# Kernel tuning notes

Hardware: AMD Instinct MI355X
Metric: run time of the kernel (lower is better)

The kernel has to match this reference:

```python
import jax, jax.numpy as jnp
import numpy as np

N_NODES = 40000
N_EDGES = 640000
IN_CH = 64
HID = 128
N_LAYERS = 3


def _linear_params(key, shape_in, shape_out):
    kw, kb = jax.random.split(key)
    lim = 1.0 / np.sqrt(shape_in)
    W = jax.random.uniform(kw, (shape_in, shape_out), jnp.float32, -lim, lim)
    b = jax.random.uniform(kb, (shape_out,), jnp.float32, -lim, lim)
    return W, b


def setup_inputs() -> dict:
    key = jax.random.key(0)
    ks = jax.random.split(key, 32)
    edge_index = jax.random.randint(ks[0], (2, N_EDGES), 0, N_NODES, dtype=jnp.int64 if jax.config.jax_enable_x64 else jnp.int32)
    x = jax.random.normal(ks[1], (N_NODES, IN_CH), jnp.float32)
    pos = jax.random.normal(ks[2], (N_NODES, 3), jnp.float32)
    emb_W, emb_b = _linear_params(ks[3], IN_CH, HID)

    def stack(fn):
        outs = [fn(l) for l in range(N_LAYERS)]
        Ws = jnp.stack([o[0] for o in outs])
        bs = jnp.stack([o[1] for o in outs])
        return Ws, bs

    # edge MLP: Linear(2H+1, H), SiLU, Linear(H, H), SiLU
    edge_W1, edge_b1 = stack(lambda l: _linear_params(ks[4 + l], 2 * HID + 1, HID))
    edge_W2, edge_b2 = stack(lambda l: _linear_params(ks[8 + l], HID, HID))
    # node MLP: Linear(2H, H), SiLU, Linear(H, H)
    node_W1, node_b1 = stack(lambda l: _linear_params(ks[12 + l], 2 * HID, HID))
    node_W2, node_b2 = stack(lambda l: _linear_params(ks[16 + l], HID, HID))
    # pos MLP: Linear(H, H), SiLU, Linear(H, 1)
    pos_W1, pos_b1 = stack(lambda l: _linear_params(ks[20 + l], HID, HID))
    pos_W2, pos_b2 = stack(lambda l: _linear_params(ks[24 + l], HID, 1))
    return {
        "edge_index": edge_index, "x": x, "pos": pos,
        "emb_W": emb_W, "emb_b": emb_b,
        "edge_W1": edge_W1, "edge_b1": edge_b1, "edge_W2": edge_W2, "edge_b2": edge_b2,
        "node_W1": node_W1, "node_b1": node_b1, "node_W2": node_W2, "node_b2": node_b2,
        "pos_W1": pos_W1, "pos_b1": pos_b1, "pos_W2": pos_W2, "pos_b2": pos_b2,
    }


def reference(edge_index, x, pos, emb_W, emb_b,
              edge_W1, edge_b1, edge_W2, edge_b2,
              node_W1, node_b1, node_W2, node_b2,
              pos_W1, pos_b1, pos_W2, pos_b2):
    silu = jax.nn.silu
    N = x.shape[0]
    src, dst = edge_index[0], edge_index[1]  # messages flow src -> dst
    # node embedding
    h = x @ emb_W + emb_b  # [N, H]
    # in-degree for mean aggregation of position updates
    deg = jnp.clip(jax.ops.segment_sum(jnp.ones(src.shape[0], pos.dtype), dst, num_segments=N), 1.0)
    L = edge_W1.shape[0]
    for l in range(L):
        h_i = h[dst]            # [E, H] target features
        h_j = h[src]            # [E, H] source features
        rel = pos[dst] - pos[src]  # [E, 3]
        d2 = jnp.sum(rel * rel, axis=-1, keepdims=True)  # [E, 1] squared distance
        e_in = jnp.concatenate([h_i, h_j, d2], axis=-1)  # [E, 2H+1]
        m = silu(silu(e_in @ edge_W1[l] + edge_b1[l]) @ edge_W2[l] + edge_b2[l])  # [E, H]
        agg = jax.ops.segment_sum(m, dst, num_segments=N)  # [N, H]
        n_in = jnp.concatenate([h, agg], axis=-1)  # [N, 2H]
        h = silu(n_in @ node_W1[l] + node_b1[l]) @ node_W2[l] + node_b2[l]
        # equivariant position update: pos_i += mean_j (pos_i - pos_j) * phi_x(m_ij)
        w = silu(m @ pos_W1[l] + pos_b1[l]) @ pos_W2[l] + pos_b2[l]  # [E, 1]
        pos = pos + jax.ops.segment_sum(rel * w, dst, num_segments=N) / deg[:, None]
    return h, pos
```

## Files before the change

### kernel.cpp

```cpp
#include <hip/hip_runtime.h>
#include <hip/hip_bf16.h>

#define N_NODES 40000
#define N_EDGES 640000
#define IN_CH 64
#define HID 128
#define N_LAYERS 3

typedef unsigned short u16;
typedef unsigned int u32;

typedef __attribute__((ext_vector_type(8))) __bf16 bf16x8;
typedef __attribute__((ext_vector_type(4))) float float4v;

__device__ __forceinline__ float bf2f(u16 u) {
    union { u32 i; float f; } v; v.i = ((u32)u) << 16; return v.f;
}
__device__ __forceinline__ float bflo(u32 p) {
    union { u32 i; float f; } v; v.i = p << 16; return v.f;
}
__device__ __forceinline__ float bfhi(u32 p) {
    union { u32 i; float f; } v; v.i = p & 0xffff0000u; return v.f;
}
__device__ __forceinline__ u16 f2bf(float f) {
    union { float f; u32 i; } v; v.f = f;
    u32 i = v.i;
    u32 r = (i + 0x7fffu + ((i >> 16) & 1u)) >> 16;
    return (u16)r;
}
#if __has_builtin(__builtin_amdgcn_cvt_pk_bf16_f32)
typedef __attribute__((ext_vector_type(2))) __bf16 bf16x2_t;
__device__ __forceinline__ u32 pk2bf(float a, float b) {
    bf16x2_t p = __builtin_amdgcn_cvt_pk_bf16_f32(a, b);
    union { bf16x2_t v; u32 u; } c; c.v = p; return c.u;
}
#else
__device__ __forceinline__ u32 pk2bf(float a, float b) {
    return (u32)f2bf(a) | ((u32)f2bf(b) << 16);
}
#endif
__device__ __forceinline__ float silu_f(float x) {
    float d = 1.0f + __expf(-x);
#if __has_builtin(__builtin_amdgcn_rcpf)
    return x * __builtin_amdgcn_rcpf(d);
#else
    return __fdividef(x, d);
#endif
}

#define W_STRIDE 72
__device__ __forceinline__ void stage_w64(const u16* __restrict__ g, u16* s, int t,
                                          int chunk, int rowstride_u32) {
    const u32* gp = (const u32*)g;
    u32* sp = (u32*)s;
#pragma unroll
    for (int it = 0; it < 4; ++it) {
        int i4 = t + it * 256;
        int n = i4 >> 3, j = i4 & 7;
        *(uint4*)(sp + n * 36 + j * 4) = *(const uint4*)(gp + n * rowstride_u32 + chunk * 32 + j * 4);
    }
}

__global__ void detect_kernel(const void* __restrict__ w_raw,
                              const void* __restrict__ eidx_raw,
                              int* __restrict__ flags) {
    __shared__ int s_big, s_hi;
    if (threadIdx.x == 0) { s_big = 0; s_hi = 0; }
    __syncthreads();
    const u16* w16 = (const u16*)w_raw;
    for (int i = threadIdx.x; i < 8192; i += blockDim.x) {
        float v = bf2f(w16[i]);
        if (!(fabsf(v) <= 1.0f)) s_big = 1;
    }
    const u32* e32 = (const u32*)eidx_raw;
    for (int i = threadIdx.x; i < 256; i += blockDim.x) {
        if (e32[2 * i + 1] != 0u) s_hi = 1;
    }
    __syncthreads();
    if (threadIdx.x == 0) {
        flags[0] = s_big ? 0 : 1;
        flags[1] = s_hi ? 0 : 1;
    }
}

__global__ void small_cvt_kernel(
    const void* __restrict__ embB_raw, const void* __restrict__ eB1_raw,
    const void* __restrict__ eB2_raw, const void* __restrict__ pB1_raw,
    const void* __restrict__ pB2_raw, const void* __restrict__ pW2_raw,
    const void* __restrict__ eW1_raw, const void* __restrict__ nB1_raw,
    const void* __restrict__ nB2_raw,
    float* __restrict__ dstf, const int* __restrict__ flags)
{
    int i = blockIdx.x * blockDim.x + threadIdx.x;
    if (i >= 2820) return;
    const void* src; int si;
    if (i < 128)       { src = embB_raw; si = i; }
    else if (i < 512)  { src = eB1_raw;  si = i - 128; }
    else if (i < 896)  { src = eB2_raw;  si = i - 512; }
    else if (i < 1280) { src = pB1_raw;  si = i - 896; }
    else if (i < 1284) { src = pB2_raw;  si = i - 1280; if (si >= 3) { dstf[i] = 0.f; return; } }
    else if (i < 1668) { src = pW2_raw;  si = i - 1284; }
    else if (i < 2052) { int j = i - 1668; src = eW1_raw; si = (j >> 7) * 32896 + 32768 + (j & 127); }
    else if (i < 2436) { src = nB1_raw;  si = i - 2052; }
    else               { src = nB2_raw;  si = i - 2436; }
    dstf[i] = flags[0] ? bf2f(((const u16*)src)[si]) : ((const float*)src)[si];
}

__global__ void wcvt_kernel(
    const void* __restrict__ eW1_raw, const void* __restrict__ eW2_raw,
    const void* __restrict__ pW1_raw, const void* __restrict__ nW1_raw,
    const void* __restrict__ nW2_raw, const void* __restrict__ embW_raw,
    u16* __restrict__ W1abt, u16* __restrict__ W2t, u16* __restrict__ pW1t,
    u16* __restrict__ nW1t, u16* __restrict__ nW2t, u16* __restrict__ embWt,
    const int* __restrict__ flags)
{
    int z = blockIdx.z, l = blockIdx.y;
    int i = blockIdx.x * blockDim.x + threadIdx.x;
    const void* src; u16* dst; int si, di;
    if (z == 0) {
        if (i >= 32768) return;
        int o = i >> 7, k = i & 127;
        si = l * 32896 + ((o < 128) ? (k * 128 + o) : ((128 + k) * 128 + (o - 128)));
        src = eW1_raw; dst = W1abt; di = l * 32768 + i;
    } else if (z == 1) {
        if (i >= 16384) return;
        int n = i >> 7, k = i & 127;
        si = l * 16384 + k * 128 + n; src = eW2_raw; dst = W2t; di = l * 16384 + i;
    } else if (z == 2) {
        if (i >= 16384) return;
        int n = i >> 7, k = i & 127;
        si = l * 16384 + k * 128 + n; src = pW1_raw; dst = pW1t; di = l * 16384 + i;
    } else if (z == 3) {
        if (i >= 32768) return;
        int n = i >> 8, k = i & 255;
        si = l * 32768 + k * 128 + n; src = nW1_raw; dst = nW1t; di = l * 32768 + i;
    } else if (z == 4) {
        if (i >= 16384) return;
        int n = i >> 7, k = i & 127;
        si = l * 16384 + k * 128 + n; src = nW2_raw; dst = nW2t; di = l * 16384 + i;
    } else {
        if (l != 0 || i >= 8192) return;
        int n = i >> 6, k = i & 63;
        si = k * 128 + n; src = embW_raw; dst = embWt; di = i;
    }
    float v = flags[0] ? bf2f(((const u16*)src)[si]) : ((const float*)src)[si];
    dst[di] = f2bf(v);
}

__global__ void cnt_kernel(const void* __restrict__ eidx, int* __restrict__ cnt,
                           const int* __restrict__ flags) {
    int e = blockIdx.x * blockDim.x + threadIdx.x;
    if (e >= N_EDGES) return;
    int dn = flags[1] ? (int)((const long long*)eidx)[N_EDGES + e]
                      : ((const int*)eidx)[N_EDGES + e];
    atomicAdd(&cnt[dn], 1);
}

__global__ __launch_bounds__(1024) void scan_kernel(const int* __restrict__ cnt,
                                                    int* __restrict__ offs) {
    __shared__ int s_part[1024];
    const int t = threadIdx.x;
    const int base = t * 40;
    int sum = 0;
    for (int j = 0; j < 40; ++j) {
        int idx = base + j;
        sum += (idx < N_NODES) ? cnt[idx] : 0;
    }
    s_part[t] = sum;
    __syncthreads();
    for (int d = 1; d < 1024; d <<= 1) {
        int v = (t >= d) ? s_part[t - d] : 0;
        __syncthreads();
        s_part[t] += v;
        __syncthreads();
    }
    int run = (t == 0) ? 0 : s_part[t - 1];
    for (int j = 0; j < 40; ++j) {
        int idx = base + j;
        if (idx < N_NODES) { offs[idx] = run; run += cnt[idx]; }
    }
    if (t == 1023) offs[N_NODES] = run;
}

__global__ void scatter_kernel(const void* __restrict__ eidx,
                               const int* __restrict__ offs, int* __restrict__ cur,
                               int* __restrict__ ssrc, int* __restrict__ sdst,
                               const int* __restrict__ flags) {
    int e = blockIdx.x * blockDim.x + threadIdx.x;
    if (e >= N_EDGES) return;
    int sn, dn;
    if (flags[1]) {
        sn = (int)((const long long*)eidx)[e];
        dn = (int)((const long long*)eidx)[N_EDGES + e];
    } else {
        sn = ((const int*)eidx)[e];
        dn = ((const int*)eidx)[N_EDGES + e];
    }
    int p = offs[dn] + atomicAdd(&cur[dn], 1);
    ssrc[p] = sn;
    sdst[p] = dn;
}

__global__ void posinit_kernel(const void* __restrict__ pos_raw, float* __restrict__ posf,
                               const int* __restrict__ flags) {
    int i = blockIdx.x * blockDim.x + threadIdx.x;
    if (i < N_NODES * 3)
        posf[i] = flags[0] ? bf2f(((const u16*)pos_raw)[i]) : ((const float*)pos_raw)[i];
}

#define ACT_STRIDE 136

__global__ __launch_bounds__(256, 3) void embed_uv_kernel(
    const void* __restrict__ x_raw, const u16* __restrict__ embWt, const float* __restrict__ embB,
    const u16* __restrict__ W1abt, const float* __restrict__ b1,
    u16* __restrict__ h, u16* __restrict__ uv, const int* __restrict__ flags)
{
    __shared__ __align__(16) u16 s_x[64 * 72];
    __shared__ __align__(16) u16 s_h[64 * ACT_STRIDE];
    __shared__ __align__(16) u16 s_w[128 * W_STRIDE];

    const int t = threadIdx.x;
    const int n0 = blockIdx.x * 64;
    const int wv = t >> 6, lane = t & 63, quad = lane >> 4, li = lane & 15;
    const int rowA = wv * 16 + li;
    const int rowC = wv * 16 + quad * 4;

    {
        int el = t >> 2, pt4 = t & 3;
        u32* op = (u32*)s_x + el * 36 + pt4 * 8;
        if (flags[0]) {
            const u32* xp = (const u32*)x_raw + (size_t)(n0 + el) * 32 + pt4 * 8;
            *(uint4*)(op)     = *(const uint4*)(xp);
            *(uint4*)(op + 4) = *(const uint4*)(xp + 4);
        } else {
            const float* xp = (const float*)x_raw + (size_t)(n0 + el) * 64 + pt4 * 16;
#pragma unroll
            for (int j = 0; j < 8; ++j) op[j] = pk2bf(xp[2 * j], xp[2 * j + 1]);
        }
    }
    stage_w64(embWt, s_w, t, 0, 32);
    __syncthreads();

    float4v acc[8];
#pragma unroll
    for (int c = 0; c < 8; ++c) {
        float bias = embB[c * 16 + li];
#pragma unroll
        for (int r = 0; r < 4; ++r) acc[c][r] = bias;
    }
#pragma unroll
    for (int kk2 = 0; kk2 < 2; ++kk2) {
        const bf16x8 av = *(const bf16x8*)(s_x + rowA * 72 + kk2 * 32 + quad * 8);
#pragma unroll
        for (int c = 0; c < 8; ++c) {
            const bf16x8 bv = *(const bf16x8*)(s_w + (c * 16 + li) * W_STRIDE + kk2 * 32 + quad * 8);
            acc[c] = __builtin_amdgcn_mfma_f32_16x16x32_bf16(av, bv, acc[c], 0, 0, 0);
        }
    }
#pragma unroll
    for (int c = 0; c < 8; ++c) {
        int col = c * 16 + li;
#pragma unroll
        for (int r = 0; r < 4; ++r) {
            float v = acc[c][r];
            float vo = __shfl_xor(v, 1, 64);
            if (!(li & 1)) {
                u32 pkd = pk2bf(v, vo);
                *(u32*)(s_h + (rowC + r) * ACT_STRIDE + col) = pkd;
                *(u32*)(h + (size_t)(n0 + rowC + r) * HID + col) = pkd;
            }
        }
    }

    float4v a2[16];
#pragma unroll
    for (int ct = 0; ct < 16; ++ct) {
        float bias = (ct < 8) ? b1[ct * 16 + li] : 0.0f;
#pragma unroll
        for (int r = 0; r < 4; ++r) a2[ct][r] = bias;
    }
#pragma unroll
    for (int half = 0; half < 2; ++half) {
#pragma unroll
        for (int chunk = 0; chunk < 2; ++chunk) {
            __syncthreads();
            stage_w64(W1abt + half * 16384, s_w, t, chunk, 64);
            __syncthreads();
#pragma unroll
            for (int kk2 = 0; kk2 < 2; ++kk2) {
                const bf16x8 av = *(const bf16x8*)(s_h + rowA * ACT_STRIDE + chunk * 64 + kk2 * 32 + quad * 8);
#pragma unroll
                for (int c = 0; c < 8; ++c) {
                    const bf16x8 bv = *(const bf16x8*)(s_w + (c * 16 + li) * W_STRIDE + kk2 * 32 + quad * 8);
                    a2[half * 8 + c] = __builtin_amdgcn_mfma_f32_16x16x32_bf16(av, bv, a2[half * 8 + c], 0, 0, 0);
                }
            }
        }
    }
#pragma unroll
    for (int ct = 0; ct < 16; ++ct) {
        int col = (ct >> 3) * 128 + (ct & 7) * 16 + li;
#pragma unroll
        for (int r = 0; r < 4; ++r) {
            float v = a2[ct][r];
            float vo = __shfl_xor(v, 1, 64);
            if (!(li & 1))
                *(u32*)(uv + (size_t)(n0 + rowC + r) * 256 + col) = pk2bf(v, vo);
        }
    }
}

#define TILE_E 64

__global__ __launch_bounds__(256, 4) void edge_mfma_kernel(
    const int* __restrict__ ssrc, const int* __restrict__ sdst,
    const u16* __restrict__ uv, const float* __restrict__ posf,
    const float* __restrict__ w1c_g,
    const u16* __restrict__ W2t, const float* __restrict__ b2,
    const u16* __restrict__ pW1t, const float* __restrict__ pb1,
    const float* __restrict__ pW2, const float* __restrict__ pb2,
    float* __restrict__ agg, float* __restrict__ pd)
{
    __shared__ __align__(16) u16 s_act[TILE_E * ACT_STRIDE];
    __shared__ __align__(16) u16 s_w[128 * W_STRIDE];
    __shared__ float s_w1c[128];
    __shared__ float s_d2[TILE_E];
    __shared__ float s_rel[TILE_E * 3];
    __shared__ int s_dstn[TILE_E];

    const int t = threadIdx.x;
    const int e0 = blockIdx.x * TILE_E;
    const int wv = t >> 6, lane = t & 63, quad = lane >> 4, li = lane & 15;
    const int rowA = wv * 16 + li;
    const int rowC = wv * 16 + quad * 4;

    {
        const int el = t >> 2, pt4 = t & 3;
        int eg = e0 + el;
        int dNg = sdst[eg], sNg = ssrc[eg];
        const uint4* up = (const uint4*)((const u32*)uv + (size_t)dNg * 128 + pt4 * 16);
        const uint4* vp = (const uint4*)((const u32*)uv + (size_t)sNg * 128 + 64 + pt4 * 16);
        uint4 uu[4], vv[4];
#pragma unroll
        for (int q4 = 0; q4 < 4; ++q4) { uu[q4] = up[q4]; vv[q4] = vp[q4]; }

        if (t < TILE_E) {
            int e = e0 + t;
            int sN = ssrc[e], dN = sdst[e];
            s_dstn[t] = dN;
            float r0 = posf[dN * 3 + 0] - posf[sN * 3 + 0];
            float r1 = posf[dN * 3 + 1] - posf[sN * 3 + 1];
            float r2 = posf[dN * 3 + 2] - posf[sN * 3 + 2];
            s_rel[t * 3 + 0] = r0; s_rel[t * 3 + 1] = r1; s_rel[t * 3 + 2] = r2;
            s_d2[t] = r0 * r0 + r1 * r1 + r2 * r2;
        }
        if (t < 128) s_w1c[t] = w1c_g[t];
        stage_w64(W2t, s_w, t, 0, 64);
        __syncthreads();

        float d2 = s_d2[el];
        u32* outp = (u32*)s_act + el * (ACT_STRIDE / 2) + pt4 * 16;
        const float* wc = s_w1c + pt4 * 32;
#pragma unroll
        for (int q4 = 0; q4 < 4; ++q4) {
            u32 res[4];
#pragma unroll
            for (int j = 0; j < 4; ++j) {
                u32 ua = ((const u32*)&uu[q4])[j], va = ((const u32*)&vv[q4])[j];
                int col = q4 * 8 + j * 2;
                float x0 = fmaf(d2, wc[col],     bflo(ua) + bflo(va));
                float x1 = fmaf(d2, wc[col + 1], bfhi(ua) + bfhi(va));
                res[j] = pk2bf(silu_f(x0), silu_f(x1));
            }
            *(uint4*)(outp + q4 * 4) = *(uint4*)res;
        }
    }
    __syncthreads();

    float4v acc[8];
#pragma unroll
    for (int c = 0; c < 8; ++c) {
        float bias = b2[c * 16 + li];
#pragma unroll
        for (int r = 0; r < 4; ++r) acc[c][r] = bias;
    }
#pragma unroll
    for (int p = 0; p < 2; ++p) {
        if (p) {
            __syncthreads();
            stage_w64(W2t, s_w, t, 1, 64);
            __syncthreads();
        }
#pragma unroll
        for (int kk2 = 0; kk2 < 2; ++kk2) {
            const bf16x8 av = *(const bf16x8*)(s_act + rowA * ACT_STRIDE + p * 64 + kk2 * 32 + quad * 8);
#pragma unroll
            for (int c = 0; c < 8; ++c) {
                const bf16x8 bv = *(const bf16x8*)(s_w + (c * 16 + li) * W_STRIDE + kk2 * 32 + quad * 8);
                acc[c] = __builtin_amdgcn_mfma_f32_16x16x32_bf16(av, bv, acc[c], 0, 0, 0);
            }
        }
    }
    __syncthreads();

#pragma unroll
    for (int c = 0; c < 8; ++c) {
        int col = c * 16 + li;
#pragma unroll
        for (int r = 0; r < 4; ++r)
            s_act[(rowC + r) * ACT_STRIDE + col] = f2bf(silu_f(acc[c][r]));
    }
    stage_w64(pW1t, s_w, t, 0, 64);
    __syncthreads();

    {
        int c32 = t & 63, grp = t >> 6;
        int r0 = grp * 16;
        float run0 = 0.f, run1 = 0.f;
        int cur = s_dstn[r0];
        for (int r = r0; r < r0 + 16; ++r) {
            int dn = s_dstn[r];
            if (dn != cur) {
                atomicAdd(&agg[(size_t)cur * HID + 2 * c32], run0);
                atomicAdd(&agg[(size_t)cur * HID + 2 * c32 + 1], run1);
                run0 = run1 = 0.f; cur = dn;
            }
            u32 mm = *((const u32*)s_act + r * (ACT_STRIDE / 2) + c32);
            run0 += bflo(mm);
            run1 += bfhi(mm);
        }
        atomicAdd(&agg[(size_t)cur * HID + 2 * c32], run0);
        atomicAdd(&agg[(size_t)cur * HID + 2 * c32 + 1], run1);
    }

#pragma unroll
    for (int c = 0; c < 8; ++c) {
        float bias = pb1[c * 16 + li];
#pragma unroll
        for (int r = 0; r < 4; ++r) acc[c][r] = bias;
    }
#pragma unroll
    for (int p = 0; p < 2; ++p) {
        if (p) {
            __syncthreads();
            stage_w64(pW1t, s_w, t, 1, 64);
            __syncthreads();
        }
#pragma unroll
        for (int kk2 = 0; kk2 < 2; ++kk2) {
            const bf16x8 av = *(const bf16x8*)(s_act + rowA * ACT_STRIDE + p * 64 + kk2 * 32 + quad * 8);
#pragma unroll
            for (int c = 0; c < 8; ++c) {
                const bf16x8 bv = *(const bf16x8*)(s_w + (c * 16 + li) * W_STRIDE + kk2 * 32 + quad * 8);
                acc[c] = __builtin_amdgcn_mfma_f32_16x16x32_bf16(av, bv, acc[c], 0, 0, 0);
            }
        }
    }
    float part[4] = {0.f, 0.f, 0.f, 0.f};
#pragma unroll
    for (int c = 0; c < 8; ++c) {
        float pw = pW2[c * 16 + li];
#pragma unroll
        for (int r = 0; r < 4; ++r) part[r] += silu_f(acc[c][r]) * pw;
    }
#pragma unroll
    for (int r = 0; r < 4; ++r) {
        part[r] += __shfl_xor(part[r], 1, 64);
        part[r] += __shfl_xor(part[r], 2, 64);
        part[r] += __shfl_xor(part[r], 4, 64);
        part[r] += __shfl_xor(part[r], 8, 64);
    }
    __syncthreads();
    if (li == 0) {
        float pb2v = pb2[0];
#pragma unroll
        for (int r = 0; r < 4; ++r) s_d2[rowC + r] = part[r] + pb2v;
    }
    __syncthreads();
    if (t < 12) {
        int a = t % 3, grp = t / 3;
        int r0 = grp * 16;
        float run = 0.f;
        int cur = s_dstn[r0];
        for (int r = r0; r < r0 + 16; ++r) {
            int dn = s_dstn[r];
            if (dn != cur) {
                atomicAdd(&pd[(size_t)cur * 3 + a], run);
                run = 0.f; cur = dn;
            }
            run += s_rel[r * 3 + a] * s_d2[r];
        }
        atomicAdd(&pd[(size_t)cur * 3 + a], run);
    }
}

#define A_STRIDE 264

__global__ __launch_bounds__(256, 3) void node_uv_kernel(
    const u16* __restrict__ h_in, float* __restrict__ agg,
    const u16* __restrict__ W1t, const float* __restrict__ b1,
    const u16* __restrict__ W2t, const float* __restrict__ b2,
    const u16* __restrict__ W1abt_nx, const float* __restrict__ b1_nx,
    u16* __restrict__ h_out, u16* __restrict__ uv,
    float* __restrict__ posf, float* __restrict__ pd, const int* __restrict__ cnt,
    void* __restrict__ outp, const int* __restrict__ flags, int do_out)
{
    __shared__ __align__(16) u16 s_a[64 * A_STRIDE];
    __shared__ __align__(16) u16 s_w[128 * W_STRIDE];

    const int t = threadIdx.x;
    const int n0 = blockIdx.x * 64;
    const int wv = t >> 6, lane = t & 63, quad = lane >> 4, li = lane & 15;
    const int rowA = wv * 16 + li;
    const int rowC = wv * 16 + quad * 4;

    {
        int nl = t >> 2, pt4 = t & 3;
        const uint4* hp = (const uint4*)((const u32*)h_in + (size_t)(n0 + nl) * 64 + pt4 * 16);
        u32* rowp = (u32*)s_a + nl * (A_STRIDE / 2) + pt4 * 16;
#pragma unroll
        for (int j = 0; j < 4; ++j) *(uint4*)(rowp + j * 4) = hp[j];
        float* ap = agg + (size_t)(n0 + nl) * HID + pt4 * 32;
        rowp += 64;
#pragma unroll
        for (int j = 0; j < 16; ++j) {
            float2 v = *(const float2*)(ap + j * 2);
            rowp[j] = pk2bf(v.x, v.y);
        }
        float4 z = {0.f, 0.f, 0.f, 0.f};
#pragma unroll
        for (int j = 0; j < 8; ++j) *(float4*)(ap + j * 4) = z;
    }
    stage_w64(W1t, s_w, t, 0, 128);
    __syncthreads();

    float4v acc[8];
#pragma unroll
    for (int c = 0; c < 8; ++c) {
        float bias = b1[c * 16 + li];
#pragma unroll
        for (int r = 0; r < 4; ++r) acc[c][r] = bias;
    }
#pragma unroll
    for (int p = 0; p < 4; ++p) {
        if (p) {
            __syncthreads();
            stage_w64(W1t, s_w, t, p, 128);
            __syncthreads();
        }
#pragma unroll
        for (int kk2 = 0; kk2 < 2; ++kk2) {
            const bf16x8 av = *(const bf16x8*)(s_a + rowA * A_STRIDE + p * 64 + kk2 * 32 + quad * 8);
#pragma unroll
            for (int c = 0; c < 8; ++c) {
                const bf16x8 bv = *(const bf16x8*)(s_w + (c * 16 + li) * W_STRIDE + kk2 * 32 + quad * 8);
                acc[c] = __builtin_amdgcn_mfma_f32_16x16x32_bf16(av, bv, acc[c], 0, 0, 0);
            }
        }
    }

    __syncthreads();
    u16* s_t1 = s_a;
#pragma unroll
    for (int c = 0; c < 8; ++c) {
        int col = c * 16 + li;
#pragma unroll
        for (int r = 0; r < 4; ++r) {
            float v = silu_f(acc[c][r]);
            float vo = __shfl_xor(v, 1, 64);
            if (!(li & 1))
                *(u32*)(s_t1 + (rowC + r) * ACT_STRIDE + col) = pk2bf(v, vo);
        }
    }
    stage_w64(W2t, s_w, t, 0, 64);
    __syncthreads();

#pragma unroll
    for (int c = 0; c < 8; ++c) {
        float bias = b2[c * 16 + li];
#pragma unroll
        for (int r = 0; r < 4; ++r) acc[c][r] = bias;
    }
#pragma unroll
    for (int p = 0; p < 2; ++p) {
        if (p) {
            __syncthreads();
            stage_w64(W2t, s_w, t, 1, 64);
            __syncthreads();
        }
#pragma unroll
        for (int kk2 = 0; kk2 < 2; ++kk2) {
            const bf16x8 av = *(const bf16x8*)(s_t1 + rowA * ACT_STRIDE + p * 64 + kk2 * 32 + quad * 8);
#pragma unroll
            for (int c = 0; c < 8; ++c) {
                const bf16x8 bv = *(const bf16x8*)(s_w + (c * 16 + li) * W_STRIDE + kk2 * 32 + quad * 8);
                acc[c] = __builtin_amdgcn_mfma_f32_16x16x32_bf16(av, bv, acc[c], 0, 0, 0);
            }
        }
    }

    if (do_out) {
        if (flags[0]) {
#pragma unroll
            for (int c = 0; c < 8; ++c) {
                int col = c * 16 + li;
#pragma unroll
                for (int r = 0; r < 4; ++r) {
                    float v = acc[c][r];
                    float vo = __shfl_xor(v, 1, 64);
                    if (!(li & 1))
                        *(u32*)((u16*)outp + (size_t)(n0 + rowC + r) * HID + col) = pk2bf(v, vo);
                }
            }
        } else {
#pragma unroll
            for (int c = 0; c < 8; ++c) {
                int col = c * 16 + li;
#pragma unroll
                for (int r = 0; r < 4; ++r)
                    ((float*)outp)[(size_t)(n0 + rowC + r) * HID + col] = acc[c][r];
            }
        }
    } else {
#pragma unroll
        for (int c = 0; c < 8; ++c) {
            int col = c * 16 + li;
#pragma unroll
            for (int r = 0; r < 4; ++r) {
                float v = acc[c][r];
                float vo = __shfl_xor(v, 1, 64);
                if (!(li & 1)) {
                    u32 pkd = pk2bf(v, vo);
                    *(u32*)(s_t1 + (rowC + r) * ACT_STRIDE + col) = pkd;
                    *(u32*)(h_out + (size_t)(n0 + rowC + r) * HID + col) = pkd;
                }
            }
        }
    }

    if (t < 192) {
        int nl = t / 3, a = t % 3;
        int n = n0 + nl;
        float dg = (float)cnt[n];
        dg = dg < 1.0f ? 1.0f : dg;
        float np = posf[n * 3 + a] + pd[n * 3 + a] / dg;
        posf[n * 3 + a] = np;
        pd[n * 3 + a] = 0.f;
        if (do_out) {
            if (flags[0]) ((u16*)outp)[(size_t)N_NODES * HID + n * 3 + a] = f2bf(np);
            else          ((float*)outp)[(size_t)N_NODES * HID + n * 3 + a] = np;
        }
    }

    if (do_out) return;

    float4v a2[16];
#pragma unroll
    for (int ct = 0; ct < 16; ++ct) {
        float bias = (ct < 8) ? b1_nx[ct * 16 + li] : 0.0f;
#pragma unroll
        for (int r = 0; r < 4; ++r) a2[ct][r] = bias;
    }
#pragma unroll
    for (int half = 0; half < 2; ++half) {
#pragma unroll
        for (int chunk = 0; chunk < 2; ++chunk) {
            __syncthreads();
            stage_w64(W1abt_nx + half * 16384, s_w, t, chunk, 64);
            __syncthreads();
#pragma unroll
            for (int kk2 = 0; kk2 < 2; ++kk2) {
                const bf16x8 av = *(const bf16x8*)(s_t1 + rowA * ACT_STRIDE + chunk * 64 + kk2 * 32 + quad * 8);
#pragma unroll
                for (int c = 0; c < 8; ++c) {
                    const bf16x8 bv = *(const bf16x8*)(s_w + (c * 16 + li) * W_STRIDE + kk2 * 32 + quad * 8);
                    a2[half * 8 + c] = __builtin_amdgcn_mfma_f32_16x16x32_bf16(av, bv, a2[half * 8 + c], 0, 0, 0);
                }
            }
        }
    }
#pragma unroll
    for (int ct = 0; ct < 16; ++ct) {
        int col = (ct >> 3) * 128 + (ct & 7) * 16 + li;
#pragma unroll
        for (int r = 0; r < 4; ++r) {
            float v = a2[ct][r];
            float vo = __shfl_xor(v, 1, 64);
            if (!(li & 1))
                *(u32*)(uv + (size_t)(n0 + rowC + r) * 256 + col) = pk2bf(v, vo);
        }
    }
}

extern "C" void kernel_launch(void* const* d_in, const int* in_sizes, int n_in,
                              void* d_out, int out_size, void* d_ws, size_t ws_size,
                              hipStream_t stream) {
    (void)in_sizes; (void)n_in; (void)out_size; (void)ws_size;

    const void* eidx_raw = d_in[0];
    const void* x_raw    = d_in[1];
    const void* pos_raw  = d_in[2];
    const void* embW_raw = d_in[3];
    const void* embB_raw = d_in[4];
    const void* eW1_raw  = d_in[5];
    const void* eB1_raw  = d_in[6];
    const void* eW2_raw  = d_in[7];
    const void* eB2_raw  = d_in[8];
    const void* nW1_raw  = d_in[9];
    const void* nB1_raw  = d_in[10];
    const void* nW2_raw  = d_in[11];
    const void* nB2_raw  = d_in[12];
    const void* pW1_raw  = d_in[13];
    const void* pB1_raw  = d_in[14];
    const void* pW2_raw  = d_in[15];
    const void* pB2_raw  = d_in[16];

    float* ws   = (float*)d_ws;
    float* posf = ws;
    float* agg  = posf + (size_t)N_NODES * 3;
    float* pd   = agg + (size_t)N_NODES * HID;
    float* smallf = pd + (size_t)N_NODES * 3;
    float* embB = smallf;
    float* eB1f = smallf + 128;
    float* eB2f = smallf + 512;
    float* pB1f = smallf + 896;
    float* pB2f = smallf + 1280;
    float* pW2f = smallf + 1284;
    float* W1r  = smallf + 1668;
    float* nB1f = smallf + 2052;
    float* nB2f = smallf + 2436;

    u16* W1abt = (u16*)(smallf + 2820);
    u16* W2t   = W1abt + 3 * 256 * 128;
    u16* pW1t  = W2t + 3 * 128 * 128;
    u16* nW1t  = pW1t + 3 * 128 * 128;
    u16* nW2t  = nW1t + 3 * 128 * 256;
    u16* embWt = nW2t + 3 * 128 * 128;
    u16* h0    = embWt + 8192;
    u16* h1    = h0 + (size_t)N_NODES * HID;
    u16* uvb   = h1 + (size_t)N_NODES * HID;
    int* ssrc  = (int*)(uvb + (size_t)N_NODES * 256);
    int* sdst  = ssrc + N_EDGES;
    int* cnt   = sdst + N_EDGES;
    int* cur   = cnt + N_NODES;
    int* offs  = cur + N_NODES;
    int* flags = offs + N_NODES + 3;

    detect_kernel<<<1, 256, 0, stream>>>(embW_raw, eidx_raw, flags);
    small_cvt_kernel<<<12, 256, 0, stream>>>(embB_raw, eB1_raw, eB2_raw, pB1_raw, pB2_raw,
                                             pW2_raw, eW1_raw, nB1_raw, nB2_raw, smallf, flags);
    wcvt_kernel<<<dim3(128, 3, 6), 256, 0, stream>>>(
        eW1_raw, eW2_raw, pW1_raw, nW1_raw, nW2_raw, embW_raw,
        W1abt, W2t, pW1t, nW1t, nW2t, embWt, flags);

    hipMemsetAsync(cnt, 0, 2 * (size_t)N_NODES * sizeof(int), stream);
    cnt_kernel<<<(N_EDGES + 255) / 256, 256, 0, stream>>>(eidx_raw, cnt, flags);
    scan_kernel<<<1, 1024, 0, stream>>>(cnt, offs);
    scatter_kernel<<<(N_EDGES + 255) / 256, 256, 0, stream>>>(eidx_raw, offs, cur, ssrc, sdst, flags);

    posinit_kernel<<<(N_NODES * 3 + 255) / 256, 256, 0, stream>>>(pos_raw, posf, flags);
    hipMemsetAsync(agg, 0, ((size_t)N_NODES * HID + (size_t)N_NODES * 3) * sizeof(float), stream);

    embed_uv_kernel<<<N_NODES / 64, 256, 0, stream>>>(x_raw, embWt, embB, W1abt, eB1f, h0, uvb, flags);

    u16* hin = h0;
    u16* hout = h1;
    for (int l = 0; l < N_LAYERS; ++l) {
        int last = (l == N_LAYERS - 1);
        edge_mfma_kernel<<<N_EDGES / TILE_E, 256, 0, stream>>>(
            ssrc, sdst, uvb, posf,
            W1r + l * HID,
            W2t + (size_t)l * 128 * 128, eB2f + l * HID,
            pW1t + (size_t)l * 128 * 128, pB1f + l * HID,
            pW2f + l * HID, pB2f + l,
            agg, pd);
        node_uv_kernel<<<N_NODES / 64, 256, 0, stream>>>(
            hin, agg,
            nW1t + (size_t)l * 128 * 256, nB1f + l * HID,
            nW2t + (size_t)l * 128 * 128, nB2f + l * HID,
            W1abt + (size_t)(last ? 0 : (l + 1)) * 32768, eB1f + (last ? 0 : (l + 1)) * HID,
            hout, uvb,
            posf, pd, cnt,
            d_out, flags, last ? 1 : 0);
        u16* tmp = hin; hin = hout; hout = tmp;
    }
}
```

Baseline: 782.6 us.

## Permute weight output columns so each lane stores contiguous 16-byte MFMA results

The transposed weight matrices are now built with a column permutation (row n maps to original column (n&15)*8 + n>>4). After this, each lane's eight MFMA accumulator tiles hold eight consecutive output columns. Epilogues can then pack them into one 16-byte store per row instead of using cross-lane shuffles and scattered 4-byte stores, and bias indexing is updated to match. This cuts shuffle and store-instruction overhead in the MLP epilogues. It relies on every consumer of the permuted weights and outputs being updated consistently.

```diff
diff --git a/kernel.cpp b/kernel.cpp
--- a/kernel.cpp
+++ b/kernel.cpp
@@ -60,6 +60,8 @@
         *(uint4*)(sp + n * 36 + j * 4) = *(const uint4*)(gp + n * rowstride_u32 + chunk * 32 + j * 4);
     }
 }
+
+__device__ __forceinline__ int permch(int r) { return ((r & 15) << 3) | (r >> 4); }
 
 __global__ void detect_kernel(const void* __restrict__ w_raw,
                               const void* __restrict__ eidx_raw,
@@ -120,12 +122,13 @@
     if (z == 0) {
         if (i >= 32768) return;
         int o = i >> 7, k = i & 127;
-        si = l * 32896 + ((o < 128) ? (k * 128 + o) : ((128 + k) * 128 + (o - 128)));
+        int ch = permch(o & 127);
+        si = l * 32896 + ((o < 128) ? (k * 128 + ch) : ((128 + k) * 128 + ch));
         src = eW1_raw; dst = W1abt; di = l * 32768 + i;
     } else if (z == 1) {
         if (i >= 16384) return;
         int n = i >> 7, k = i & 127;
-        si = l * 16384 + k * 128 + n; src = eW2_raw; dst = W2t; di = l * 16384 + i;
+        si = l * 16384 + k * 128 + permch(n); src = eW2_raw; dst = W2t; di = l * 16384 + i;
     } else if (z == 2) {
         if (i >= 16384) return;
         int n = i >> 7, k = i & 127;
@@ -133,15 +136,15 @@
     } else if (z == 3) {
         if (i >= 32768) return;
         int n = i >> 8, k = i & 255;
-        si = l * 32768 + k * 128 + n; src = nW1_raw; dst = nW1t; di = l * 32768 + i;
+        si = l * 32768 + k * 128 + permch(n); src = nW1_raw; dst = nW1t; di = l * 32768 + i;
     } else if (z == 4) {
         if (i >= 16384) return;
         int n = i >> 7, k = i & 127;
-        si = l * 16384 + k * 128 + n; src = nW2_raw; dst = nW2t; di = l * 16384 + i;
+        si = l * 16384 + k * 128 + permch(n); src = nW2_raw; dst = nW2t; di = l * 16384 + i;
     } else {
         if (l != 0 || i >= 8192) return;
         int n = i >> 6, k = i & 63;
-        si = k * 128 + n; src = embW_raw; dst = embWt; di = i;
+        si = k * 128 + permch(n); src = embW_raw; dst = embWt; di = i;
     }
     float v = flags[0] ? bf2f(((const u16*)src)[si]) : ((const float*)src)[si];
     dst[di] = f2bf(v);
@@ -244,7 +247,7 @@
     float4v acc[8];
 #pragma unroll
     for (int c = 0; c < 8; ++c) {
-        float bias = embB[c * 16 + li];
+        float bias = embB[li * 8 + c];
 #pragma unroll
         for (int r = 0; r < 4; ++r) acc[c][r] = bias;
     }
@@ -258,24 +261,19 @@
         }
     }
 #pragma unroll
-    for (int c = 0; c < 8; ++c) {
-        int col = c * 16 + li;
-#pragma unroll
-        for (int r = 0; r < 4; ++r) {
-            float v = acc[c][r];
-            float vo = __shfl_xor(v, 1, 64);
-            if (!(li & 1)) {
-                u32 pkd = pk2bf(v, vo);
-                *(u32*)(s_h + (rowC + r) * ACT_STRIDE + col) = pkd;
-                *(u32*)(h + (size_t)(n0 + rowC + r) * HID + col) = pkd;
-            }
-        }
+    for (int r = 0; r < 4; ++r) {
+        u32 res[4];
+#pragma unroll
+        for (int c2 = 0; c2 < 4; ++c2)
+            res[c2] = pk2bf(acc[2 * c2][r], acc[2 * c2 + 1][r]);
+        *(uint4*)((u32*)s_h + (rowC + r) * (ACT_STRIDE / 2) + li * 4) = *(uint4*)res;
+        *(uint4*)((u32*)h + (size_t)(n0 + rowC + r) * 64 + li * 4) = *(uint4*)res;
     }
 
     float4v a2[16];
 #pragma unroll
     for (int ct = 0; ct < 16; ++ct) {
-        float bias = (ct < 8) ? b1[ct * 16 + li] : 0.0f;
+        float bias = (ct < 8) ? b1[li * 8 + ct] : 0.0f;
 #pragma unroll
         for (int r = 0; r < 4; ++r) a2[ct][r] = bias;
     }
@@ -298,14 +296,14 @@
         }
     }
 #pragma unroll
-    for (int ct = 0; ct < 16; ++ct) {
-        int col = (ct >> 3) * 128 + (ct & 7) * 16 + li;
+    for (int half = 0; half < 2; ++half) {
 #pragma unroll
         for (int r = 0; r < 4; ++r) {
-            float v = a2[ct][r];
-            float vo = __shfl_xor(v, 1, 64);
-            if (!(li & 1))
-                *(u32*)(uv + (size_t)(n0 + rowC + r) * 256 + col) = pk2bf(v, vo);
+            u32 res[4];
+#pragma unroll
+            for (int c2 = 0; c2 < 4; ++c2)
+                res[c2] = pk2bf(a2[half * 8 + 2 * c2][r], a2[half * 8 + 2 * c2 + 1][r]);
+            *(uint4*)((u32*)uv + (size_t)(n0 + rowC + r) * 128 + half * 64 + li * 4) = *(uint4*)res;
         }
     }
 }
@@ -380,7 +378,7 @@
     float4v acc[8];
 #pragma unroll
     for (int c = 0; c < 8; ++c) {
-        float bias = b2[c * 16 + li];
+        float bias = b2[li * 8 + c];
 #pragma unroll
         for (int r = 0; r < 4; ++r) acc[c][r] = bias;
     }
@@ -404,11 +402,12 @@
     __syncthreads();
 
 #pragma unroll
-    for (int c = 0; c < 8; ++c) {
-        int col = c * 16 + li;
-#pragma unroll
-        for (int r = 0; r < 4; ++r)
-            s_act[(rowC + r) * ACT_STRIDE + col] = f2bf(silu_f(acc[c][r]));
+    for (int r = 0; r < 4; ++r) {
+        u32 res[4];
+#pragma unroll
+        for (int c2 = 0; c2 < 4; ++c2)
+            res[c2] = pk2bf(silu_f(acc[2 * c2][r]), silu_f(acc[2 * c2 + 1][r]));
+        *(uint4*)((u32*)s_act + (rowC + r) * (ACT_STRIDE / 2) + li * 4) = *(uint4*)res;
     }
     stage_w64(pW1t, s_w, t, 0, 64);
     __syncthreads();
@@ -537,7 +536,7 @@
     float4v acc[8];
 #pragma unroll
     for (int c = 0; c < 8; ++c) {
-        float bias = b1[c * 16 + li];
+        float bias = b1[li * 8 + c];
 #pragma unroll
         for (int r = 0; r < 4; ++r) acc[c][r] = bias;
     }
@@ -562,22 +561,19 @@
     __syncthreads();
     u16* s_t1 = s_a;
 #pragma unroll
+    for (int r = 0; r < 4; ++r) {
+        u32 res[4];
+#pragma unroll
+        for (int c2 = 0; c2 < 4; ++c2)
+            res[c2] = pk2bf(silu_f(acc[2 * c2][r]), silu_f(acc[2 * c2 + 1][r]));
+        *(uint4*)((u32*)s_t1 + (rowC + r) * (ACT_STRIDE / 2) + li * 4) = *(uint4*)res;
+    }
+    stage_w64(W2t, s_w, t, 0, 64);
+    __syncthreads();
+
+#pragma unroll
     for (int c = 0; c < 8; ++c) {
-        int col = c * 16 + li;
-#pragma unroll
-        for (int r = 0; r < 4; ++r) {
-            float v = silu_f(acc[c][r]);
-            float vo = __shfl_xor(v, 1, 64);
-            if (!(li & 1))
-                *(u32*)(s_t1 + (rowC + r) * ACT_STRIDE + col) = pk2bf(v, vo);
-        }
-    }
-    stage_w64(W2t, s_w, t, 0, 64);
-    __syncthreads();
-
-#pragma unroll
-    for (int c = 0; c < 8; ++c) {
-        float bias = b2[c * 16 + li];
+        float bias = b2[li * 8 + c];
 #pragma unroll
         for (int r = 0; r < 4; ++r) acc[c][r] = bias;
     }
@@ -602,39 +598,32 @@
     if (do_out) {
         if (flags[0]) {
 #pragma unroll
-            for (int c = 0; c < 8; ++c) {
-                int col = c * 16 + li;
-#pragma unroll
-                for (int r = 0; r < 4; ++r) {
-                    float v = acc[c][r];
-                    float vo = __shfl_xor(v, 1, 64);
-                    if (!(li & 1))
-                        *(u32*)((u16*)outp + (size_t)(n0 + rowC + r) * HID + col) = pk2bf(v, vo);
-                }
+            for (int r = 0; r < 4; ++r) {
+                u32 res[4];
+#pragma unroll
+                for (int c2 = 0; c2 < 4; ++c2)
+                    res[c2] = pk2bf(acc[2 * c2][r], acc[2 * c2 + 1][r]);
+                *(uint4*)((u32*)outp + (size_t)(n0 + rowC + r) * 64 + li * 4) = *(uint4*)res;
             }
         } else {
 #pragma unroll
-            for (int c = 0; c < 8; ++c) {
-                int col = c * 16 + li;
-#pragma unroll
-                for (int r = 0; r < 4; ++r)
-                    ((float*)outp)[(size_t)(n0 + rowC + r) * HID + col] = acc[c][r];
+            for (int r = 0; r < 4; ++r) {
+                float* op = (float*)outp + (size_t)(n0 + rowC + r) * HID + li * 8;
+                float4 lo = {acc[0][r], acc[1][r], acc[2][r], acc[3][r]};
+                float4 hi = {acc[4][r], acc[5][r], acc[6][r], acc[7][r]};
+                *(float4*)op = lo;
+                *(float4*)(op + 4) = hi;
             }
         }
     } else {
 #pragma unroll
-        for (int c = 0; c < 8; ++c) {
-            int col = c * 16 + li;
-#pragma unroll
-            for (int r = 0; r < 4; ++r) {
-                float v = acc[c][r];
-                float vo = __shfl_xor(v, 1, 64);
-                if (!(li & 1)) {
-                    u32 pkd = pk2bf(v, vo);
-                    *(u32*)(s_t1 + (rowC + r) * ACT_STRIDE + col) = pkd;
-                    *(u32*)(h_out + (size_t)(n0 + rowC + r) * HID + col) = pkd;
-                }
-            }
+        for (int r = 0; r < 4; ++r) {
+            u32 res[4];
+#pragma unroll
+            for (int c2 = 0; c2 < 4; ++c2)
+                res[c2] = pk2bf(acc[2 * c2][r], acc[2 * c2 + 1][r]);
+            *(uint4*)((u32*)s_t1 + (rowC + r) * (ACT_STRIDE / 2) + li * 4) = *(uint4*)res;
+            *(uint4*)((u32*)h_out + (size_t)(n0 + rowC + r) * 64 + li * 4) = *(uint4*)res;
         }
     }
 
@@ -657,7 +646,7 @@
     float4v a2[16];
 #pragma unroll
     for (int ct = 0; ct < 16; ++ct) {
-        float bias = (ct < 8) ? b1_nx[ct * 16 + li] : 0.0f;
+        float bias = (ct < 8) ? b1_nx[li * 8 + ct] : 0.0f;
 #pragma unroll
         for (int r = 0; r < 4; ++r) a2[ct][r] = bias;
     }
@@ -680,14 +669,14 @@
         }
     }
 #pragma unroll
-    for (int ct = 0; ct < 16; ++ct) {
-        int col = (ct >> 3) * 128 + (ct & 7) * 16 + li;
+    for (int half = 0; half < 2; ++half) {
 #pragma unroll
         for (int r = 0; r < 4; ++r) {
-            float v = a2[ct][r];
-            float vo = __shfl_xor(v, 1, 64);
-            if (!(li & 1))
-                *(u32*)(uv + (size_t)(n0 + rowC + r) * 256 + col) = pk2bf(v, vo);
+            u32 res[4];
+#pragma unroll
+            for (int c2 = 0; c2 < 4; ++c2)
+                res[c2] = pk2bf(a2[half * 8 + 2 * c2][r], a2[half * 8 + 2 * c2 + 1][r]);
+            *(uint4*)((u32*)uv + (size_t)(n0 + rowC + r) * 128 + half * 64 + li * 4) = *(uint4*)res;
         }
     }
 }
```

Result: no change. 768.7 us (-1.8%).
